# Kernel optimization log

Measured on AMD Instinct MI355X. Metric: run time of the kernel, lower is better.

## Reference

```python
import jax, jax.numpy as jnp
import numpy as np

E = 768      # embed_dim
H = 12       # num_heads
DH = E // H  # head_dim = 64
L = 128      # tgt_len
B = 2        # bsz
NEG_SLOPE = 0.01  # F.leaky_relu default


def setup_inputs() -> dict:
    key = jax.random.key(0)
    ks = jax.random.split(key, 18)
    s = 0.02
    w = lambda k, shape: jax.random.normal(k, shape, dtype=jnp.float32) * s
    return {
        'query': jax.random.normal(ks[0], (L, B, E), dtype=jnp.float32),
        'entity': jax.random.normal(ks[1], (L, B, E), dtype=jnp.float32),
        # Conv1d(E, E, kernel_size=2, padding=1): weight (out, in, 2)
        'conv_w': w(ks[2], (E, E, 2)), 'conv_b': w(ks[3], (E,)),
        # Linear(E, E//2) projections: weight (out, in)
        'q_w': w(ks[4], (E // 2, E)), 'q_b': w(ks[5], (E // 2,)),
        'k_w': w(ks[6], (E // 2, E)), 'k_b': w(ks[7], (E // 2,)),
        'v_w': w(ks[8], (E // 2, E)), 'v_b': w(ks[9], (E // 2,)),
        'e_w': w(ks[10], (E // 2, E)), 'e_b': w(ks[11], (E // 2,)),
        # attn_fc: Linear(3*head_dim, 1)
        'attn_w': w(ks[12], (1, 3 * DH)), 'attn_b': w(ks[13], (1,)),
        # ConvTranspose1d(E, E, kernel_size=2): weight (in, out, 2)
        'deconv_w': w(ks[14], (E, E, 2)), 'deconv_b': w(ks[15], (E,)),
        'out_w': w(ks[16], (E, E)), 'out_b': w(ks[17], (E,)),
    }


def _prev(x):
    # x shifted by one along time (zero-padded at t=0): x_prev[t] = x[t-1]
    return jnp.concatenate([jnp.zeros_like(x[:1]), x[:-1]], axis=0)


def _forward(query, entity, conv_w, conv_b, q_w, q_b, k_w, k_b, v_w, v_b,
             e_w, e_b, attn_w, attn_b, deconv_w, deconv_b, out_w, out_b):
    Lq, Bq, _ = query.shape
    BH = Bq * H
    lin = lambda x, W, b: x @ W.T + b

    # conv1D(query) with padding=1, then slice [:, :, :L]:
    # out[t] = W[:,:,0] @ x[t-1] + W[:,:,1] @ x[t] + b   (x[-1] = 0)
    nq = (jnp.einsum('oi,lbi->lbo', conv_w[:, :, 0], _prev(query)) +
          jnp.einsum('oi,lbi->lbo', conv_w[:, :, 1], query) + conv_b)

    e = lin(entity, e_w, e_b)           # (L, B, E/2)
    q = lin(nq, q_w, q_b)
    k = lin(nq, k_w, k_b)               # self-attention: k, v from conv'd query
    v = lin(nq, v_w, v_b)

    # _shape: view(L, B*H, Dh).transpose(0, 1) -> (B*H, L, Dh)
    shp = lambda t: t.reshape(Lq, BH, DH).transpose(1, 0, 2)
    qe = shp(jnp.concatenate([q, e], axis=-1))
    ke = shp(jnp.concatenate([k, e], axis=-1))
    ve = shp(jnp.concatenate([v, e], axis=-1))

    # edge[i, j, b] = entity[i, b] - entity[j, b]; then raw row-major view
    # (L, L, B, E) -> (B*H, L, L, Dh), exactly matching torch .contiguous().view
    edge = (entity[:, None] - entity[None, :]).reshape(BH, Lq, Lq, DH)

    # qe: transpose(0,1).repeat(L,1,1,1).transpose(0,1).reshape(BH, L, L, Dh)
    # yields T[x, y, m, d] = qe[m, x, d], then raw row-major reshape
    qe_big = jnp.broadcast_to(qe.transpose(1, 0, 2)[:, None],
                              (Lq, Lq, BH, DH)).reshape(BH, Lq, Lq, DH)
    # ke: repeat(L,1,1,1).reshape -> R[a, m, l, d] = ke[m, l, d], raw reshape
    ke_big = jnp.broadcast_to(ke[None], (Lq, BH, Lq, DH)).reshape(BH, Lq, Lq, DH)

    # attn_fc(cat([qe, ke, edge], -1)).squeeze() as three partial dots
    wv = attn_w[0]
    scores = (jnp.einsum('bijd,d->bij', qe_big, wv[:DH]) +
              jnp.einsum('bijd,d->bij', ke_big, wv[DH:2 * DH]) +
              jnp.einsum('bijd,d->bij', edge, wv[2 * DH:]) + attn_b[0])
    scores = jnp.where(scores >= 0, scores, NEG_SLOPE * scores)  # leaky_relu

    probs = jax.nn.softmax(scores, axis=-1)  # dropout p=0 -> no-op
    attn = jnp.einsum('bij,bjd->bid', probs, ve)          # (B*H, L, Dh)
    a = attn.transpose(1, 0, 2).reshape(Lq, Bq, E)        # (L, B, E)

    # deconv1D (ConvTranspose1d k=2), slice [:, :, :L]:
    # out[t] = W[:,:,0]^T x[t] + W[:,:,1]^T x[t-1] + b
    y = (jnp.einsum('io,lbi->lbo', deconv_w[:, :, 0], a) +
         jnp.einsum('io,lbi->lbo', deconv_w[:, :, 1], _prev(a)) + deconv_b)

    return lin(y, out_w, out_b)


def reference(query, entity, conv_w, conv_b, q_w, q_b, k_w, k_b, v_w, v_b,
              e_w, e_b, attn_w, attn_b, deconv_w, deconv_b, out_w, out_b):
    return _forward(query, entity, conv_w, conv_b, q_w, q_b, k_w, k_b,
                    v_w, v_b, e_w, e_b, attn_w, attn_b, deconv_w, deconv_b,
                    out_w, out_b)
```

## Files before the change

kernel.cpp:

```cpp
#include <hip/hip_runtime.h>

#define ASS 34
#define BSS 68

__device__ inline float wsum(float v) {
#pragma unroll
  for (int off = 32; off; off >>= 1) v += __shfl_xor(v, off, 64);
  return v;
}

struct P {
  const float *query, *entity, *conv_w, *conv_b, *q_w, *q_b, *k_w, *k_b;
  const float *v_w, *v_b, *e_w, *e_b, *attn_w, *attn_b, *deconv_w, *deconv_b;
  const float *out_w, *out_b;
  float *nq0, *nq1, *nq2, *nq3, *e_buf, *v_buf, *qw_red, *kw_red, *qb_red, *kb_red;
  float *Abuf, *Bkbuf, *Ewbuf, *a_buf, *y, *dout;
};

template <int TAPMODE, bool ATOMIC>
__device__ __forceinline__ void conv_v2(const float* __restrict__ A,
                                        const float* __restrict__ W,
                                        float* __restrict__ C,
                                        int m0, int n0, int kbase, int ktiles,
                                        float* smem) {
  float* AsB  = smem;
  float* Bs0B = smem + 2 * 32 * ASS;
  float* Bs1B = Bs0B + 2 * 32 * BSS;
  const int tid = threadIdx.x;
  const int ar = tid >> 3, ak4 = (tid & 7) << 2;
  const int gmA = m0 - 2 + ar;
  const bool extra = (tid < 16);
  const int ar2 = 32 + (tid >> 3);
  const int gmA2 = m0 + 30 + (tid >> 3);
  const int tn = tid & 15, tm = tid >> 4;
  const int bn = tid >> 2, ig = tid & 3;
  const int il = tid >> 3, ng = tid & 7;

  float4 pa, pa2, pb[4];
  auto ld = [&](int t) {
    int gi = kbase + t * 32;
    pa = (gmA >= 0) ? *(const float4*)(A + (size_t)gmA * 768 + gi + ak4)
                    : make_float4(0.f, 0.f, 0.f, 0.f);
    if (extra) pa2 = *(const float4*)(A + (size_t)gmA2 * 768 + gi + ak4);
    if (TAPMODE == 0) {
      const float* wrow = W + (size_t)(n0 + bn) * 1536 + 2 * (gi + ig * 8);
#pragma unroll
      for (int c = 0; c < 4; ++c) pb[c] = *(const float4*)(wrow + 4 * c);
    } else {
      const float* wrow = W + (size_t)(gi + il) * 1536 + 2 * (n0 + ng * 8);
#pragma unroll
      for (int c = 0; c < 4; ++c) pb[c] = *(const float4*)(wrow + 4 * c);
    }
  };

  ld(0);
  float acc[2][4] = {};
  for (int t = 0; t < ktiles; ++t) {
    float* As  = AsB + (t & 1) * (32 * ASS);
    float* Bs0 = Bs0B + (t & 1) * (32 * BSS);
    float* Bs1 = Bs1B + (t & 1) * (32 * BSS);
#pragma unroll
    for (int c = 0; c < 4; ++c) {
      float v = (c == 0) ? pa.x : (c == 1) ? pa.y : (c == 2) ? pa.z : pa.w;
      As[(ak4 + c) * ASS + ar] = v;
    }
    if (extra) {
#pragma unroll
      for (int c = 0; c < 4; ++c) {
        float v = (c == 0) ? pa2.x : (c == 1) ? pa2.y : (c == 2) ? pa2.z : pa2.w;
        As[(ak4 + c) * ASS + ar2] = v;
      }
    }
    if (TAPMODE == 0) {
#pragma unroll
      for (int c = 0; c < 4; ++c) {
        int i_l = ig * 8 + 2 * c;
        Bs0[i_l * BSS + bn] = pb[c].x; Bs1[i_l * BSS + bn] = pb[c].y;
        Bs0[(i_l + 1) * BSS + bn] = pb[c].z; Bs1[(i_l + 1) * BSS + bn] = pb[c].w;
      }
    } else {
#pragma unroll
      for (int c = 0; c < 4; ++c) {
        int n_l = ng * 8 + 2 * c;
        Bs0[il * BSS + n_l] = pb[c].x; Bs1[il * BSS + n_l] = pb[c].y;
        Bs0[il * BSS + n_l + 1] = pb[c].z; Bs1[il * BSS + n_l + 1] = pb[c].w;
      }
    }
    __syncthreads();
    if (t + 1 < ktiles) ld(t + 1);
#pragma unroll
    for (int i = 0; i < 32; ++i) {
      float4 b0 = *(const float4*)(Bs0 + i * BSS + (tn << 2));
      float4 b1 = *(const float4*)(Bs1 + i * BSS + (tn << 2));
      float ap0 = As[i * ASS + (tm << 1)];
      float ap1 = As[i * ASS + (tm << 1) + 1];
      float ac0 = As[i * ASS + (tm << 1) + 2];
      float ac1 = As[i * ASS + (tm << 1) + 3];
      float bc[4] = {b0.x, b0.y, b0.z, b0.w};
      float bp[4] = {b1.x, b1.y, b1.z, b1.w};
#pragma unroll
      for (int jj = 0; jj < 4; ++jj) {
        if (TAPMODE == 0) {
          acc[0][jj] += ac0 * bp[jj] + ap0 * bc[jj];
          acc[1][jj] += ac1 * bp[jj] + ap1 * bc[jj];
        } else {
          acc[0][jj] += ac0 * bc[jj] + ap0 * bp[jj];
          acc[1][jj] += ac1 * bc[jj] + ap1 * bp[jj];
        }
      }
    }
  }
#pragma unroll
  for (int j = 0; j < 2; ++j) {
    int m = m0 + (tm << 1) + j;
    if (ATOMIC) {
#pragma unroll
      for (int jj = 0; jj < 4; ++jj)
        unsafeAtomicAdd(&C[(size_t)m * 768 + n0 + (tn << 2) + jj], acc[j][jj]);
    } else {
      float4 o = make_float4(acc[j][0], acc[j][1], acc[j][2], acc[j][3]);
      *(float4*)(C + (size_t)m * 768 + n0 + (tn << 2)) = o;
    }
  }
}

template <int NSUM, bool ATOMIC>
__device__ __forceinline__ void gemm_v2(const float* __restrict__ A0,
                                        const float* __restrict__ A1,
                                        const float* __restrict__ A2,
                                        const float* __restrict__ A3,
                                        const float* __restrict__ arow,
                                        const float* __restrict__ Bw,
                                        const float* __restrict__ bias,
                                        float* __restrict__ C, int N,
                                        int m0, int n0, int kbase, int ktiles,
                                        float* smem) {
  float* AsB = smem;
  float* BsB = smem + 2 * 32 * ASS;
  const int tid = threadIdx.x;
  const int ar = tid >> 3, ak4 = (tid & 7) << 2;
  const int br = tid >> 2, bk4 = (tid & 3) << 2;
  const int tn = tid & 15, tm = tid >> 4;
  const float* Brow = Bw + (size_t)(n0 + br) * 768;
  float4 pa, pb0, pb1;
  auto ld = [&](int t) {
    int gi = kbase + t * 32;
    size_t ao = (size_t)(m0 + ar) * 768 + gi + ak4;
    pa = *(const float4*)(A0 + ao);
    if constexpr (NSUM == 4) {
      float4 t1 = *(const float4*)(A1 + ao);
      float4 t2 = *(const float4*)(A2 + ao);
      float4 t3 = *(const float4*)(A3 + ao);
      float4 t4 = *(const float4*)(arow + gi + ak4);
      pa.x += t1.x + t2.x + t3.x + t4.x;
      pa.y += t1.y + t2.y + t3.y + t4.y;
      pa.z += t1.z + t2.z + t3.z + t4.z;
      pa.w += t1.w + t2.w + t3.w + t4.w;
    }
    pb0 = *(const float4*)(Brow + gi + bk4);
    pb1 = *(const float4*)(Brow + gi + bk4 + 16);
  };
  ld(0);
  float acc[2][4] = {};
  for (int t = 0; t < ktiles; ++t) {
    float* As = AsB + (t & 1) * (32 * ASS);
    float* Bs = BsB + (t & 1) * (32 * BSS);
    As[(ak4 + 0) * ASS + ar] = pa.x; As[(ak4 + 1) * ASS + ar] = pa.y;
    As[(ak4 + 2) * ASS + ar] = pa.z; As[(ak4 + 3) * ASS + ar] = pa.w;
    Bs[(bk4 + 0) * BSS + br] = pb0.x; Bs[(bk4 + 1) * BSS + br] = pb0.y;
    Bs[(bk4 + 2) * BSS + br] = pb0.z; Bs[(bk4 + 3) * BSS + br] = pb0.w;
    Bs[(bk4 + 16) * BSS + br] = pb1.x; Bs[(bk4 + 17) * BSS + br] = pb1.y;
    Bs[(bk4 + 18) * BSS + br] = pb1.z; Bs[(bk4 + 19) * BSS + br] = pb1.w;
    __syncthreads();
    if (t + 1 < ktiles) ld(t + 1);
#pragma unroll
    for (int k = 0; k < 32; ++k) {
      float a0 = As[k * ASS + (tm << 1)];
      float a1 = As[k * ASS + (tm << 1) + 1];
      float4 b4 = *(const float4*)(Bs + k * BSS + (tn << 2));
      float bb[4] = {b4.x, b4.y, b4.z, b4.w};
#pragma unroll
      for (int jj = 0; jj < 4; ++jj) {
        acc[0][jj] += a0 * bb[jj];
        acc[1][jj] += a1 * bb[jj];
      }
    }
  }
#pragma unroll
  for (int i = 0; i < 2; ++i) {
    int m = m0 + (tm << 1) + i;
    if (ATOMIC) {
#pragma unroll
      for (int jj = 0; jj < 4; ++jj)
        unsafeAtomicAdd(&C[(size_t)m * N + n0 + (tn << 2) + jj], acc[i][jj]);
    } else {
      const float* bp = bias + n0 + (tn << 2);
      float4 o = make_float4(acc[i][0] + bp[0], acc[i][1] + bp[1],
                             acc[i][2] + bp[2], acc[i][3] + bp[3]);
      *(float4*)(C + (size_t)m * N + n0 + (tn << 2)) = o;
    }
  }
}

__global__ __launch_bounds__(256) void s1(P p) {
  __shared__ float smem[2 * 32 * ASS + 4 * 32 * BSS];
  const int bid = blockIdx.x, tid = threadIdx.x;
  const int wv4 = tid >> 6, lane = tid & 63;
  if (bid < 384) {
    int kz = bid & 3, t = bid >> 2;
    float* dst = (kz == 0) ? p.nq0 : (kz == 1) ? p.nq1 : (kz == 2) ? p.nq2 : p.nq3;
    conv_v2<0, false>(p.query, p.conv_w, dst, (t / 12) * 32, (t % 12) * 64,
                      kz * 192, 6, smem);
  } else if (bid < 432) {
    int t = bid - 384;
    gemm_v2<0, false>(p.entity, nullptr, nullptr, nullptr, nullptr, p.e_w, p.e_b,
                      p.e_buf, 384, (t / 6) * 32, (t % 6) * 64, 0, 24, smem);
  } else if (bid < 472) {
    int W = (bid - 432) * 4 + wv4;
    if (W < 72) {
      int h = W / 12, ib = W % 12, i = ib * 64 + lane;
      float s = 0.f;
#pragma unroll 8
      for (int d = 0; d < 64; ++d) s += p.q_w[(h * 64 + d) * 768 + i] * p.attn_w[d];
      p.qw_red[h * 768 + i] = s;
    } else if (W < 144) {
      int r = W - 72;
      int h = r / 12, ib = r % 12, i = ib * 64 + lane;
      float s = 0.f;
#pragma unroll 8
      for (int d = 0; d < 64; ++d) s += p.k_w[(h * 64 + d) * 768 + i] * p.attn_w[64 + d];
      p.kw_red[h * 768 + i] = s;
    } else if (W < 156) {
      int r = W - 144;
      if (r < 6) {
        float s = wsum(p.q_b[r * 64 + lane] * p.attn_w[lane]);
        if (lane == 0) p.qb_red[r] = s;
      } else {
        float s = wsum(p.k_b[(r - 6) * 64 + lane] * p.attn_w[64 + lane]);
        if (lane == 0) p.kb_red[r - 6] = s;
      }
    }
  } else if (bid < 536) {
    int row = (bid - 472) * 4 + wv4;
    const float* erow = p.entity + (size_t)row * 768;
    float wvl = p.attn_w[128 + lane];
#pragma unroll
    for (int cb = 0; cb < 12; ++cb) {
      float s = wsum(erow[cb * 64 + lane] * wvl);
      if (lane == 0) p.Ewbuf[row * 12 + cb] = s;
    }
  } else {
    int iv = (bid - 536) * 256 + tid;
    const float4* vb4 = (const float4*)p.v_b;
    const float4* db4 = (const float4*)p.deconv_b;
    const float4* ob4 = (const float4*)p.out_b;
    float4* v4 = (float4*)p.v_buf;
    float4* y4 = (float4*)p.y;
    float4* o4 = (float4*)p.dout;
#pragma unroll
    for (int s = 0; s < 16; ++s) {
      int f = s * 7680 + iv;
      if (f < 24576) {
        v4[f] = vb4[f % 96];
      } else if (f < 73728) {
        int j = f - 24576;
        y4[j] = db4[j % 192];
      } else {
        int j = f - 73728;
        o4[j] = ob4[j % 192];
      }
    }
  }
}

__global__ __launch_bounds__(256) void s2(P p) {
  __shared__ float smem[2 * 32 * ASS + 2 * 32 * BSS];
  const int bid = blockIdx.x, tid = threadIdx.x;
  if (bid < 192) {
    int kz = bid & 3, t = bid >> 2;
    gemm_v2<4, true>(p.nq0, p.nq1, p.nq2, p.nq3, p.conv_b, p.v_w, nullptr,
                     p.v_buf, 384, (t / 6) * 32, (t % 6) * 64, kz * 192, 6, smem);
    return;
  }
  int wave = (bid - 192) * 4 + (tid >> 6);
  int lane = tid & 63;
  for (int W = wave; W < 6144; W += 1536) {
    if (W < 1536) {
      int x = W & 127, q = W >> 7;
      int b = q / 6, h = q % 6;
      const size_t row = (size_t)(x * 2 + b) * 768;
      const float* ww = p.qw_red + h * 768;
      float pacc = 0.f;
#pragma unroll
      for (int it = 0; it < 12; ++it) {
        int i = it * 64 + lane;
        float nv = p.nq0[row + i] + p.nq1[row + i] + p.nq2[row + i] +
                   p.nq3[row + i] + p.conv_b[i];
        pacc += nv * ww[i];
      }
      float s = wsum(pacc) + p.qb_red[h];
      if (lane == 0) p.Abuf[(b * 12 + h) * 128 + x] = s;
    } else if (W < 3072) {
      int r = W - 1536;
      int x = r & 127, q = r >> 7;
      int b = q / 6, he = q % 6;
      float s = wsum(p.e_buf[(size_t)(x * 2 + b) * 384 + he * 64 + lane] * p.attn_w[lane]);
      if (lane == 0) p.Abuf[(b * 12 + 6 + he) * 128 + x] = s;
    } else if (W < 4608) {
      int r = W - 3072;
      int l = r & 127, q = r >> 7;
      int b = q / 6, h = q % 6;
      const size_t row = (size_t)(l * 2 + b) * 768;
      const float* ww = p.kw_red + h * 768;
      float pacc = 0.f;
#pragma unroll
      for (int it = 0; it < 12; ++it) {
        int i = it * 64 + lane;
        float nv = p.nq0[row + i] + p.nq1[row + i] + p.nq2[row + i] +
                   p.nq3[row + i] + p.conv_b[i];
        pacc += nv * ww[i];
      }
      float s = wsum(pacc) + p.kb_red[h];
      if (lane == 0) p.Bkbuf[(b * 12 + h) * 128 + l] = s;
    } else {
      int r = W - 4608;
      int l = r & 127, q = r >> 7;
      int b = q / 6, he = q % 6;
      float s = wsum(p.e_buf[(size_t)(l * 2 + b) * 384 + he * 64 + lane] * p.attn_w[64 + lane]);
      if (lane == 0) p.Bkbuf[(b * 12 + 6 + he) * 128 + l] = s;
    }
  }
}

__global__ __launch_bounds__(256) void s3(P p) {
  __shared__ float smem[520];
  float* ps   = smem;
  float* redm = smem + 256;
  float* reds = smem + 260;
  float* pv   = smem + 264;
  const int tid = threadIdx.x;
  const int half = tid >> 7;
  const int t = tid & 127;
  const int widx = (tid >> 6) & 1;
  const int lane = tid & 63;
  const float ab0 = p.attn_b[0];

  int u = blockIdx.x * 2 + half;
  int bh = u >> 7, i2 = u & 127;
  int j = t;
  int G = u * 128 + j;
  int mq = G % 24, xq = (G / 24) >> 7;
  int mk = u % 24;
  int cb = G % 12, gb = G / 12;
  int be = gb & 1, ij = gb >> 1, ie = ij >> 7, je = ij & 127;
  float s = p.Abuf[mq * 128 + xq] + p.Bkbuf[mk * 128 + j] +
            p.Ewbuf[ie * 24 + be * 12 + cb] - p.Ewbuf[je * 24 + be * 12 + cb] + ab0;
  s = s >= 0.f ? s : 0.01f * s;

  float mv = s;
#pragma unroll
  for (int off = 32; off; off >>= 1) mv = fmaxf(mv, __shfl_xor(mv, off, 64));
  if (lane == 0) redm[half * 2 + widx] = mv;
  __syncthreads();
  float gmax = fmaxf(redm[half * 2], redm[half * 2 + 1]);
  float ex = expf(s - gmax);
  float sv = wsum(ex);
  if (lane == 0) reds[half * 2 + widx] = sv;
  __syncthreads();
  float gsum = reds[half * 2] + reds[half * 2 + 1];
  ps[half * 128 + t] = ex / gsum;
  __syncthreads();

  int d = t & 63, jh = t >> 6;
  int b = bh / 12, h = bh % 12;
  const float* src = (h < 6) ? (p.v_buf + h * 64) : (p.e_buf + (h - 6) * 64);
  float acc = 0.f;
#pragma unroll 8
  for (int jj = 0; jj < 64; ++jj) {
    int jx = jh * 64 + jj;
    acc += ps[half * 128 + jx] * src[(size_t)(jx * 2 + b) * 384 + d];
  }
  pv[half * 128 + jh * 64 + d] = acc;
  __syncthreads();
  if (t < 64) {
    p.a_buf[(size_t)(i2 * 2 + b) * 768 + h * 64 + t] =
        pv[half * 128 + t] + pv[half * 128 + 64 + t];
  }
}

__global__ __launch_bounds__(256) void s4(P p) {
  __shared__ float smem[2 * 32 * ASS + 4 * 32 * BSS];
  int kz = blockIdx.x & 3, t = blockIdx.x >> 2;
  conv_v2<1, true>(p.a_buf, p.deconv_w, p.y, (t / 12) * 32, (t % 12) * 64,
                   kz * 192, 6, smem);
}

__global__ __launch_bounds__(256) void s5(P p) {
  __shared__ float smem[2 * 32 * ASS + 2 * 32 * BSS];
  int kz = blockIdx.x & 3, t = blockIdx.x >> 2;
  gemm_v2<0, true>(p.y, nullptr, nullptr, nullptr, nullptr, p.out_w, nullptr,
                   p.dout, 768, (t / 12) * 32, (t % 12) * 64, kz * 192, 6, smem);
}

extern "C" void kernel_launch(void* const* d_in, const int* in_sizes, int n_in,
                              void* d_out, int out_size, void* d_ws, size_t ws_size,
                              hipStream_t stream) {
  P p;
  p.query    = (const float*)d_in[0];
  p.entity   = (const float*)d_in[1];
  p.conv_w   = (const float*)d_in[2];
  p.conv_b   = (const float*)d_in[3];
  p.q_w      = (const float*)d_in[4];
  p.q_b      = (const float*)d_in[5];
  p.k_w      = (const float*)d_in[6];
  p.k_b      = (const float*)d_in[7];
  p.v_w      = (const float*)d_in[8];
  p.v_b      = (const float*)d_in[9];
  p.e_w      = (const float*)d_in[10];
  p.e_b      = (const float*)d_in[11];
  p.attn_w   = (const float*)d_in[12];
  p.attn_b   = (const float*)d_in[13];
  p.deconv_w = (const float*)d_in[14];
  p.deconv_b = (const float*)d_in[15];
  p.out_w    = (const float*)d_in[16];
  p.out_b    = (const float*)d_in[17];

  float* ws = (float*)d_ws;
  p.nq0    = ws;
  p.nq1    = p.nq0 + 196608;
  p.nq2    = p.nq1 + 196608;
  p.nq3    = p.nq2 + 196608;
  p.e_buf  = p.nq3 + 196608;
  p.v_buf  = p.e_buf + 98304;
  p.qw_red = p.v_buf + 98304;
  p.kw_red = p.qw_red + 4608;
  p.qb_red = p.kw_red + 4608;
  p.kb_red = p.qb_red + 8;
  p.Abuf   = p.kb_red + 8;
  p.Bkbuf  = p.Abuf + 3072;
  p.Ewbuf  = p.Bkbuf + 3072;
  p.a_buf  = p.Ewbuf + 3072;
  p.y      = p.a_buf + 196608;
  p.dout   = (float*)d_out;

  s1<<<566, 256, 0, stream>>>(p);
  s2<<<576, 256, 0, stream>>>(p);
  s3<<<1536, 256, 0, stream>>>(p);
  s4<<<384, 256, 0, stream>>>(p);
  s5<<<384, 256, 0, stream>>>(p);
}
```

Before: 184.8 us.

## Fold output projection into deconv weights and merge final two GEMM stages

Each call now precomputes M0/M1 = out_w composed with the two deconv taps, plus the folded bias out_w·deconv_b, inside the first kernel. The separate deconv and output GEMM kernels then collapse into a single two-tap GEMM on the attention output, which removes one launch and the y intermediate buffer. The conv split-K drops from four partial buffers to two, so downstream consumers sum fewer partials. In exchange, the weight-fold GEMM (768x768x768, two taps) adds more arithmetic per call than the activation GEMMs it replaces, and it lengthens the first kernel.

```diff
diff --git a/kernel.cpp b/kernel.cpp
--- a/kernel.cpp
+++ b/kernel.cpp
@@ -13,11 +13,10 @@
   const float *query, *entity, *conv_w, *conv_b, *q_w, *q_b, *k_w, *k_b;
   const float *v_w, *v_b, *e_w, *e_b, *attn_w, *attn_b, *deconv_w, *deconv_b;
   const float *out_w, *out_b;
-  float *nq0, *nq1, *nq2, *nq3, *e_buf, *v_buf, *qw_red, *kw_red, *qb_red, *kb_red;
-  float *Abuf, *Bkbuf, *Ewbuf, *a_buf, *y, *dout;
+  float *nq0, *nq1, *e_buf, *v_buf, *qw_red, *kw_red, *qb_red, *kb_red;
+  float *Abuf, *Bkbuf, *Ewbuf, *a_buf, *M0, *M1, *b2db, *dout;
 };
 
-template <int TAPMODE, bool ATOMIC>
 __device__ __forceinline__ void conv_v2(const float* __restrict__ A,
                                         const float* __restrict__ W,
                                         float* __restrict__ C,
@@ -34,7 +33,6 @@
   const int gmA2 = m0 + 30 + (tid >> 3);
   const int tn = tid & 15, tm = tid >> 4;
   const int bn = tid >> 2, ig = tid & 3;
-  const int il = tid >> 3, ng = tid & 7;
 
   float4 pa, pa2, pb[4];
   auto ld = [&](int t) {
@@ -42,15 +40,9 @@
     pa = (gmA >= 0) ? *(const float4*)(A + (size_t)gmA * 768 + gi + ak4)
                     : make_float4(0.f, 0.f, 0.f, 0.f);
     if (extra) pa2 = *(const float4*)(A + (size_t)gmA2 * 768 + gi + ak4);
-    if (TAPMODE == 0) {
-      const float* wrow = W + (size_t)(n0 + bn) * 1536 + 2 * (gi + ig * 8);
-#pragma unroll
-      for (int c = 0; c < 4; ++c) pb[c] = *(const float4*)(wrow + 4 * c);
-    } else {
-      const float* wrow = W + (size_t)(gi + il) * 1536 + 2 * (n0 + ng * 8);
-#pragma unroll
-      for (int c = 0; c < 4; ++c) pb[c] = *(const float4*)(wrow + 4 * c);
-    }
+    const float* wrow = W + (size_t)(n0 + bn) * 1536 + 2 * (gi + ig * 8);
+#pragma unroll
+    for (int c = 0; c < 4; ++c) pb[c] = *(const float4*)(wrow + 4 * c);
   };
 
   ld(0);
@@ -71,20 +63,11 @@
         As[(ak4 + c) * ASS + ar2] = v;
       }
     }
-    if (TAPMODE == 0) {
-#pragma unroll
-      for (int c = 0; c < 4; ++c) {
-        int i_l = ig * 8 + 2 * c;
-        Bs0[i_l * BSS + bn] = pb[c].x; Bs1[i_l * BSS + bn] = pb[c].y;
-        Bs0[(i_l + 1) * BSS + bn] = pb[c].z; Bs1[(i_l + 1) * BSS + bn] = pb[c].w;
-      }
-    } else {
-#pragma unroll
-      for (int c = 0; c < 4; ++c) {
-        int n_l = ng * 8 + 2 * c;
-        Bs0[il * BSS + n_l] = pb[c].x; Bs1[il * BSS + n_l] = pb[c].y;
-        Bs0[il * BSS + n_l + 1] = pb[c].z; Bs1[il * BSS + n_l + 1] = pb[c].w;
-      }
+#pragma unroll
+    for (int c = 0; c < 4; ++c) {
+      int i_l = ig * 8 + 2 * c;
+      Bs0[i_l * BSS + bn] = pb[c].x; Bs1[i_l * BSS + bn] = pb[c].y;
+      Bs0[(i_l + 1) * BSS + bn] = pb[c].z; Bs1[(i_l + 1) * BSS + bn] = pb[c].w;
     }
     __syncthreads();
     if (t + 1 < ktiles) ld(t + 1);
@@ -100,35 +83,22 @@
       float bp[4] = {b1.x, b1.y, b1.z, b1.w};
 #pragma unroll
       for (int jj = 0; jj < 4; ++jj) {
-        if (TAPMODE == 0) {
-          acc[0][jj] += ac0 * bp[jj] + ap0 * bc[jj];
-          acc[1][jj] += ac1 * bp[jj] + ap1 * bc[jj];
-        } else {
-          acc[0][jj] += ac0 * bc[jj] + ap0 * bp[jj];
-          acc[1][jj] += ac1 * bc[jj] + ap1 * bp[jj];
-        }
+        acc[0][jj] += ac0 * bp[jj] + ap0 * bc[jj];
+        acc[1][jj] += ac1 * bp[jj] + ap1 * bc[jj];
       }
     }
   }
 #pragma unroll
   for (int j = 0; j < 2; ++j) {
     int m = m0 + (tm << 1) + j;
-    if (ATOMIC) {
-#pragma unroll
-      for (int jj = 0; jj < 4; ++jj)
-        unsafeAtomicAdd(&C[(size_t)m * 768 + n0 + (tn << 2) + jj], acc[j][jj]);
-    } else {
-      float4 o = make_float4(acc[j][0], acc[j][1], acc[j][2], acc[j][3]);
-      *(float4*)(C + (size_t)m * 768 + n0 + (tn << 2)) = o;
-    }
+    float4 o = make_float4(acc[j][0], acc[j][1], acc[j][2], acc[j][3]);
+    *(float4*)(C + (size_t)m * 768 + n0 + (tn << 2)) = o;
   }
 }
 
 template <int NSUM, bool ATOMIC>
 __device__ __forceinline__ void gemm_v2(const float* __restrict__ A0,
                                         const float* __restrict__ A1,
-                                        const float* __restrict__ A2,
-                                        const float* __restrict__ A3,
                                         const float* __restrict__ arow,
                                         const float* __restrict__ Bw,
                                         const float* __restrict__ bias,
@@ -147,15 +117,11 @@
     int gi = kbase + t * 32;
     size_t ao = (size_t)(m0 + ar) * 768 + gi + ak4;
     pa = *(const float4*)(A0 + ao);
-    if constexpr (NSUM == 4) {
+    if constexpr (NSUM == 2) {
       float4 t1 = *(const float4*)(A1 + ao);
-      float4 t2 = *(const float4*)(A2 + ao);
-      float4 t3 = *(const float4*)(A3 + ao);
       float4 t4 = *(const float4*)(arow + gi + ak4);
-      pa.x += t1.x + t2.x + t3.x + t4.x;
-      pa.y += t1.y + t2.y + t3.y + t4.y;
-      pa.z += t1.z + t2.z + t3.z + t4.z;
-      pa.w += t1.w + t2.w + t3.w + t4.w;
+      pa.x += t1.x + t4.x; pa.y += t1.y + t4.y;
+      pa.z += t1.z + t4.z; pa.w += t1.w + t4.w;
     }
     pb0 = *(const float4*)(Brow + gi + bk4);
     pb1 = *(const float4*)(Brow + gi + bk4 + 16);
@@ -202,21 +168,169 @@
   }
 }
 
+__device__ __forceinline__ void mfold_core(const float* __restrict__ ow,
+                                           const float* __restrict__ dw,
+                                           float* __restrict__ M0,
+                                           float* __restrict__ M1,
+                                           int n0, int i0, float* smem) {
+  float* AsB  = smem;
+  float* Bs0B = smem + 2 * 32 * ASS;
+  float* Bs1B = Bs0B + 2 * 32 * BSS;
+  const int tid = threadIdx.x;
+  const int ar = tid >> 3, ak4 = (tid & 7) << 2;
+  const int bn = tid >> 2, ig = tid & 3;
+  const int tn = tid & 15, tm = tid >> 4;
+  float4 pa, pb[4];
+  auto ld = [&](int t) {
+    int gi = t * 32;
+    pa = *(const float4*)(ow + (size_t)(n0 + ar) * 768 + gi + ak4);
+    const float* wrow = dw + (size_t)(i0 + bn) * 1536 + 2 * (gi + ig * 8);
+#pragma unroll
+    for (int c = 0; c < 4; ++c) pb[c] = *(const float4*)(wrow + 4 * c);
+  };
+  ld(0);
+  float acc0[2][4] = {}, acc1[2][4] = {};
+  for (int t = 0; t < 24; ++t) {
+    float* As  = AsB + (t & 1) * (32 * ASS);
+    float* Bs0 = Bs0B + (t & 1) * (32 * BSS);
+    float* Bs1 = Bs1B + (t & 1) * (32 * BSS);
+    As[(ak4 + 0) * ASS + ar] = pa.x; As[(ak4 + 1) * ASS + ar] = pa.y;
+    As[(ak4 + 2) * ASS + ar] = pa.z; As[(ak4 + 3) * ASS + ar] = pa.w;
+#pragma unroll
+    for (int c = 0; c < 4; ++c) {
+      int i_l = ig * 8 + 2 * c;
+      Bs0[i_l * BSS + bn] = pb[c].x; Bs1[i_l * BSS + bn] = pb[c].y;
+      Bs0[(i_l + 1) * BSS + bn] = pb[c].z; Bs1[(i_l + 1) * BSS + bn] = pb[c].w;
+    }
+    __syncthreads();
+    if (t + 1 < 24) ld(t + 1);
+#pragma unroll
+    for (int o = 0; o < 32; ++o) {
+      float a0 = As[o * ASS + (tm << 1)];
+      float a1 = As[o * ASS + (tm << 1) + 1];
+      float4 b0 = *(const float4*)(Bs0 + o * BSS + (tn << 2));
+      float4 b1 = *(const float4*)(Bs1 + o * BSS + (tn << 2));
+      float c0[4] = {b0.x, b0.y, b0.z, b0.w};
+      float c1[4] = {b1.x, b1.y, b1.z, b1.w};
+#pragma unroll
+      for (int jj = 0; jj < 4; ++jj) {
+        acc0[0][jj] += a0 * c0[jj]; acc0[1][jj] += a1 * c0[jj];
+        acc1[0][jj] += a0 * c1[jj]; acc1[1][jj] += a1 * c1[jj];
+      }
+    }
+  }
+#pragma unroll
+  for (int j = 0; j < 2; ++j) {
+    int n = n0 + (tm << 1) + j;
+    *(float4*)(M0 + (size_t)n * 768 + i0 + (tn << 2)) =
+        make_float4(acc0[j][0], acc0[j][1], acc0[j][2], acc0[j][3]);
+    *(float4*)(M1 + (size_t)n * 768 + i0 + (tn << 2)) =
+        make_float4(acc1[j][0], acc1[j][1], acc1[j][2], acc1[j][3]);
+  }
+}
+
+__device__ __forceinline__ void mm2_core(const float* __restrict__ A,
+                                         const float* __restrict__ M0,
+                                         const float* __restrict__ M1,
+                                         const float* __restrict__ b2db,
+                                         float* __restrict__ C,
+                                         int m0, int n0, int kbase, int ktiles,
+                                         bool addb, float* smem) {
+  float* AsB  = smem;
+  float* Bs0B = smem + 2 * 32 * ASS;
+  float* Bs1B = Bs0B + 2 * 32 * BSS;
+  const int tid = threadIdx.x;
+  const int ar = tid >> 3, ak4 = (tid & 7) << 2;
+  const int gmA = m0 - 2 + ar;
+  const bool extra = (tid < 16);
+  const int ar2 = 32 + (tid >> 3);
+  const int gmA2 = m0 + 30 + (tid >> 3);
+  const int br = tid >> 2, bk4 = (tid & 3) << 2;
+  const int tn = tid & 15, tm = tid >> 4;
+  float4 pa, pa2, pb00, pb01, pb10, pb11;
+  auto ld = [&](int t) {
+    int gi = kbase + t * 32;
+    pa = (gmA >= 0) ? *(const float4*)(A + (size_t)gmA * 768 + gi + ak4)
+                    : make_float4(0.f, 0.f, 0.f, 0.f);
+    if (extra) pa2 = *(const float4*)(A + (size_t)gmA2 * 768 + gi + ak4);
+    const float* r0 = M0 + (size_t)(n0 + br) * 768 + gi;
+    const float* r1 = M1 + (size_t)(n0 + br) * 768 + gi;
+    pb00 = *(const float4*)(r0 + bk4); pb01 = *(const float4*)(r0 + bk4 + 16);
+    pb10 = *(const float4*)(r1 + bk4); pb11 = *(const float4*)(r1 + bk4 + 16);
+  };
+  ld(0);
+  float acc[2][4] = {};
+  for (int t = 0; t < ktiles; ++t) {
+    float* As  = AsB + (t & 1) * (32 * ASS);
+    float* Bs0 = Bs0B + (t & 1) * (32 * BSS);
+    float* Bs1 = Bs1B + (t & 1) * (32 * BSS);
+#pragma unroll
+    for (int c = 0; c < 4; ++c) {
+      float v = (c == 0) ? pa.x : (c == 1) ? pa.y : (c == 2) ? pa.z : pa.w;
+      As[(ak4 + c) * ASS + ar] = v;
+    }
+    if (extra) {
+#pragma unroll
+      for (int c = 0; c < 4; ++c) {
+        float v = (c == 0) ? pa2.x : (c == 1) ? pa2.y : (c == 2) ? pa2.z : pa2.w;
+        As[(ak4 + c) * ASS + ar2] = v;
+      }
+    }
+    Bs0[(bk4 + 0) * BSS + br] = pb00.x; Bs0[(bk4 + 1) * BSS + br] = pb00.y;
+    Bs0[(bk4 + 2) * BSS + br] = pb00.z; Bs0[(bk4 + 3) * BSS + br] = pb00.w;
+    Bs0[(bk4 + 16) * BSS + br] = pb01.x; Bs0[(bk4 + 17) * BSS + br] = pb01.y;
+    Bs0[(bk4 + 18) * BSS + br] = pb01.z; Bs0[(bk4 + 19) * BSS + br] = pb01.w;
+    Bs1[(bk4 + 0) * BSS + br] = pb10.x; Bs1[(bk4 + 1) * BSS + br] = pb10.y;
+    Bs1[(bk4 + 2) * BSS + br] = pb10.z; Bs1[(bk4 + 3) * BSS + br] = pb10.w;
+    Bs1[(bk4 + 16) * BSS + br] = pb11.x; Bs1[(bk4 + 17) * BSS + br] = pb11.y;
+    Bs1[(bk4 + 18) * BSS + br] = pb11.z; Bs1[(bk4 + 19) * BSS + br] = pb11.w;
+    __syncthreads();
+    if (t + 1 < ktiles) ld(t + 1);
+#pragma unroll
+    for (int i = 0; i < 32; ++i) {
+      float4 b0 = *(const float4*)(Bs0 + i * BSS + (tn << 2));
+      float4 b1 = *(const float4*)(Bs1 + i * BSS + (tn << 2));
+      float ap0 = As[i * ASS + (tm << 1)];
+      float ap1 = As[i * ASS + (tm << 1) + 1];
+      float ac0 = As[i * ASS + (tm << 1) + 2];
+      float ac1 = As[i * ASS + (tm << 1) + 3];
+      float c0[4] = {b0.x, b0.y, b0.z, b0.w};
+      float c1[4] = {b1.x, b1.y, b1.z, b1.w};
+#pragma unroll
+      for (int jj = 0; jj < 4; ++jj) {
+        acc[0][jj] += ac0 * c0[jj] + ap0 * c1[jj];
+        acc[1][jj] += ac1 * c0[jj] + ap1 * c1[jj];
+      }
+    }
+  }
+#pragma unroll
+  for (int j = 0; j < 2; ++j) {
+    int m = m0 + (tm << 1) + j;
+#pragma unroll
+    for (int jj = 0; jj < 4; ++jj) {
+      float v = acc[j][jj] + (addb ? b2db[n0 + (tn << 2) + jj] : 0.f);
+      unsafeAtomicAdd(&C[(size_t)m * 768 + n0 + (tn << 2) + jj], v);
+    }
+  }
+}
+
 __global__ __launch_bounds__(256) void s1(P p) {
   __shared__ float smem[2 * 32 * ASS + 4 * 32 * BSS];
   const int bid = blockIdx.x, tid = threadIdx.x;
   const int wv4 = tid >> 6, lane = tid & 63;
-  if (bid < 384) {
-    int kz = bid & 3, t = bid >> 2;
-    float* dst = (kz == 0) ? p.nq0 : (kz == 1) ? p.nq1 : (kz == 2) ? p.nq2 : p.nq3;
-    conv_v2<0, false>(p.query, p.conv_w, dst, (t / 12) * 32, (t % 12) * 64,
-                      kz * 192, 6, smem);
-  } else if (bid < 432) {
-    int t = bid - 384;
-    gemm_v2<0, false>(p.entity, nullptr, nullptr, nullptr, nullptr, p.e_w, p.e_b,
-                      p.e_buf, 384, (t / 6) * 32, (t % 6) * 64, 0, 24, smem);
-  } else if (bid < 472) {
-    int W = (bid - 432) * 4 + wv4;
+  if (bid < 192) {
+    int kz = bid & 1, t = bid >> 1;
+    conv_v2(p.query, p.conv_w, kz ? p.nq1 : p.nq0, (t / 12) * 32, (t % 12) * 64,
+            kz * 384, 12, smem);
+  } else if (bid < 240) {
+    int t = bid - 192;
+    gemm_v2<0, false>(p.entity, nullptr, nullptr, p.e_w, p.e_b, p.e_buf, 384,
+                      (t / 6) * 32, (t % 6) * 64, 0, 24, smem);
+  } else if (bid < 528) {
+    int t = bid - 240;
+    mfold_core(p.out_w, p.deconv_w, p.M0, p.M1, (t / 12) * 32, (t % 12) * 64, smem);
+  } else if (bid < 568) {
+    int W = (bid - 528) * 4 + wv4;
     if (W < 72) {
       int h = W / 12, ib = W % 12, i = ib * 64 + lane;
       float s = 0.f;
@@ -240,8 +354,8 @@
         if (lane == 0) p.kb_red[r - 6] = s;
       }
     }
-  } else if (bid < 536) {
-    int row = (bid - 472) * 4 + wv4;
+  } else if (bid < 632) {
+    int row = (bid - 568) * 4 + wv4;
     const float* erow = p.entity + (size_t)row * 768;
     float wvl = p.attn_w[128 + lane];
 #pragma unroll
@@ -249,27 +363,28 @@
       float s = wsum(erow[cb * 64 + lane] * wvl);
       if (lane == 0) p.Ewbuf[row * 12 + cb] = s;
     }
-  } else {
-    int iv = (bid - 536) * 256 + tid;
+  } else if (bid < 704) {
+    int iv = (bid - 632) * 256 + tid;
     const float4* vb4 = (const float4*)p.v_b;
-    const float4* db4 = (const float4*)p.deconv_b;
     const float4* ob4 = (const float4*)p.out_b;
     float4* v4 = (float4*)p.v_buf;
-    float4* y4 = (float4*)p.y;
     float4* o4 = (float4*)p.dout;
 #pragma unroll
-    for (int s = 0; s < 16; ++s) {
-      int f = s * 7680 + iv;
-      if (f < 24576) {
-        v4[f] = vb4[f % 96];
-      } else if (f < 73728) {
-        int j = f - 24576;
-        y4[j] = db4[j % 192];
-      } else {
-        int j = f - 73728;
-        o4[j] = ob4[j % 192];
-      }
-    }
+    for (int s = 0; s < 4; ++s) {
+      int f = s * 18432 + iv;
+      if (f < 24576) v4[f] = vb4[f % 96];
+      else { int j = f - 24576; o4[j] = ob4[j % 192]; }
+    }
+  } else {
+    float* dbs = smem;
+    for (int i = tid; i < 768; i += 256) dbs[i] = p.deconv_b[i];
+    __syncthreads();
+    int n = (bid - 704) * 256 + tid;
+    const float* row = p.out_w + (size_t)n * 768;
+    float s = 0.f;
+#pragma unroll 8
+    for (int o = 0; o < 768; ++o) s += row[o] * dbs[o];
+    p.b2db[n] = s;
   }
 }
 
@@ -278,8 +393,8 @@
   const int bid = blockIdx.x, tid = threadIdx.x;
   if (bid < 192) {
     int kz = bid & 3, t = bid >> 2;
-    gemm_v2<4, true>(p.nq0, p.nq1, p.nq2, p.nq3, p.conv_b, p.v_w, nullptr,
-                     p.v_buf, 384, (t / 6) * 32, (t % 6) * 64, kz * 192, 6, smem);
+    gemm_v2<2, true>(p.nq0, p.nq1, p.conv_b, p.v_w, nullptr, p.v_buf, 384,
+                     (t / 6) * 32, (t % 6) * 64, kz * 192, 6, smem);
     return;
   }
   int wave = (bid - 192) * 4 + (tid >> 6);
@@ -294,9 +409,7 @@
 #pragma unroll
       for (int it = 0; it < 12; ++it) {
         int i = it * 64 + lane;
-        float nv = p.nq0[row + i] + p.nq1[row + i] + p.nq2[row + i] +
-                   p.nq3[row + i] + p.conv_b[i];
-        pacc += nv * ww[i];
+        pacc += (p.nq0[row + i] + p.nq1[row + i] + p.conv_b[i]) * ww[i];
       }
       float s = wsum(pacc) + p.qb_red[h];
       if (lane == 0) p.Abuf[(b * 12 + h) * 128 + x] = s;
@@ -316,9 +429,7 @@
 #pragma unroll
       for (int it = 0; it < 12; ++it) {
         int i = it * 64 + lane;
-        float nv = p.nq0[row + i] + p.nq1[row + i] + p.nq2[row + i] +
-                   p.nq3[row + i] + p.conv_b[i];
-        pacc += nv * ww[i];
+        pacc += (p.nq0[row + i] + p.nq1[row + i] + p.conv_b[i]) * ww[i];
       }
       float s = wsum(pacc) + p.kb_red[h];
       if (lane == 0) p.Bkbuf[(b * 12 + h) * 128 + l] = s;
@@ -390,16 +501,9 @@
 
 __global__ __launch_bounds__(256) void s4(P p) {
   __shared__ float smem[2 * 32 * ASS + 4 * 32 * BSS];
-  int kz = blockIdx.x & 3, t = blockIdx.x >> 2;
-  conv_v2<1, true>(p.a_buf, p.deconv_w, p.y, (t / 12) * 32, (t % 12) * 64,
-                   kz * 192, 6, smem);
-}
-
-__global__ __launch_bounds__(256) void s5(P p) {
-  __shared__ float smem[2 * 32 * ASS + 2 * 32 * BSS];
-  int kz = blockIdx.x & 3, t = blockIdx.x >> 2;
-  gemm_v2<0, true>(p.y, nullptr, nullptr, nullptr, nullptr, p.out_w, nullptr,
-                   p.dout, 768, (t / 12) * 32, (t % 12) * 64, kz * 192, 6, smem);
+  int kz = blockIdx.x & 1, t = blockIdx.x >> 1;
+  mm2_core(p.a_buf, p.M0, p.M1, p.b2db, p.dout, (t / 12) * 32, (t % 12) * 64,
+           kz * 384, 12, kz == 0, smem);
 }
 
 extern "C" void kernel_launch(void* const* d_in, const int* in_sizes, int n_in,
@@ -428,9 +532,7 @@
   float* ws = (float*)d_ws;
   p.nq0    = ws;
   p.nq1    = p.nq0 + 196608;
-  p.nq2    = p.nq1 + 196608;
-  p.nq3    = p.nq2 + 196608;
-  p.e_buf  = p.nq3 + 196608;
+  p.e_buf  = p.nq1 + 196608;
   p.v_buf  = p.e_buf + 98304;
   p.qw_red = p.v_buf + 98304;
   p.kw_red = p.qw_red + 4608;
@@ -440,12 +542,13 @@
   p.Bkbuf  = p.Abuf + 3072;
   p.Ewbuf  = p.Bkbuf + 3072;
   p.a_buf  = p.Ewbuf + 3072;
-  p.y      = p.a_buf + 196608;
+  p.M0     = p.a_buf + 196608;
+  p.M1     = p.M0 + 589824;
+  p.b2db   = p.M1 + 589824;
   p.dout   = (float*)d_out;
 
-  s1<<<566, 256, 0, stream>>>(p);
+  s1<<<707, 256, 0, stream>>>(p);
   s2<<<576, 256, 0, stream>>>(p);
   s3<<<1536, 256, 0, stream>>>(p);
-  s4<<<384, 256, 0, stream>>>(p);
-  s5<<<384, 256, 0, stream>>>(p);
-}
+  s4<<<192, 256, 0, stream>>>(p);
+}
```

Measured after the change: 218.6 us. 1.18x slower.
